# Kernel tuning notes

Measured on AMD Instinct MI355X. Metric: run time of the kernel, lower is better.

Reference implementation:

```python
import jax, jax.numpy as jnp
import numpy as np

VARIANCE = (0.1, 0.2)   # SSD variance from init_kwargs
TOP_K = 1000            # max detections / NMS candidates per (image, class)


def _pairwise_iou(b):
    # b: [K,4] in point form (x1,y1,x2,y2)
    area = jnp.maximum(b[:, 2] - b[:, 0], 0.0) * jnp.maximum(b[:, 3] - b[:, 1], 0.0)
    lt = jnp.maximum(b[:, None, :2], b[None, :, :2])
    rb = jnp.minimum(b[:, None, 2:], b[None, :, 2:])
    wh = jnp.maximum(rb - lt, 0.0)
    inter = wh[..., 0] * wh[..., 1]
    union = area[:, None] + area[None, :] - inter
    return inter / jnp.maximum(union, 1e-12)


def _nms_pack(points, csboxes, scores, conf_thresh, nms_thresh):
    # points/csboxes: [P,4]; scores: [P]. Returns [TOP_K, 5] = (score, cx, cy, w, h)
    K = TOP_K
    masked = jnp.where(scores >= conf_thresh, scores, -jnp.inf)
    vals, idx = jax.lax.top_k(masked, K)          # sorted descending
    p = points[idx]                                # [K,4] point form
    cs = csboxes[idx]                              # [K,4] center-size form
    valid = vals >= conf_thresh
    iou = _pairwise_iou(p)                         # [K,K]
    ar = jnp.arange(K)

    def body(i, keep):
        # box i (if kept) suppresses all lower-scored boxes with IoU > thresh
        sup = (iou[i] > nms_thresh) & (ar > i) & keep[i]
        return keep & ~sup

    keep = jax.lax.fori_loop(0, K, body, valid)
    rows = jnp.concatenate([vals[:, None], cs], axis=1)        # [K,5]
    pos = jnp.where(keep, jnp.cumsum(keep) - 1, K)             # compact kept rows to front
    out = jnp.zeros((K, 5), rows.dtype).at[pos].set(rows, mode='drop')
    return out


def setup_inputs() -> dict:
    key = jax.random.key(0)
    k1, k2, k3, k4 = jax.random.split(key, 4)
    B, P, C = 8, 120000, 5
    loc_data = jax.random.normal(k1, (B, 4, P), dtype=jnp.float32) * 0.5
    conf_data = jax.random.normal(k2, (B, C, P), dtype=jnp.float32)
    cxcy = jax.random.uniform(k3, (P, 2), dtype=jnp.float32)
    wh = 0.01 + 0.29 * jax.random.uniform(k4, (P, 2), dtype=jnp.float32)
    prior_data = jnp.concatenate([cxcy, wh], axis=1)           # (cx,cy,w,h) in [0,1]
    return {
        'loc_data': loc_data,
        'conf_data': conf_data,
        'prior_data': prior_data,
        'conf_thresh': jnp.float32(0.05),
        'nms_thresh': jnp.float32(0.5),
    }


def reference(loc_data, conf_data, prior_data, conf_thresh, nms_thresh):
    v0, v1 = VARIANCE
    # softmax over class dim, drop background class 0 -> [B, Cfg, P]
    conf = jax.nn.softmax(conf_data, axis=1)[:, 1:]
    loc = jnp.transpose(loc_data, (0, 2, 1))                   # [B,P,4]
    # SSD decode -> center-size boxes
    cxcy = prior_data[None, :, :2] + loc[..., :2] * v0 * prior_data[None, :, 2:]
    wh = prior_data[None, :, 2:] * jnp.exp(loc[..., 2:] * v1)
    cs = jnp.concatenate([cxcy, wh], axis=-1)                  # [B,P,4] center-size
    pts = jnp.concatenate([cxcy - wh / 2, cxcy + wh / 2], axis=-1)  # [B,P,4] point form
    per_class = jax.vmap(_nms_pack, in_axes=(None, None, 0, None, None))
    per_image = jax.vmap(per_class, in_axes=(0, 0, 0, None, None))
    return per_image(pts, cs, conf, conf_thresh, nms_thresh)   # [B, Cfg, TOP_K, 5]
```

## Files before the change

kernel.cpp:

```cpp
#include <hip/hip_runtime.h>
#include <cstdint>
#include <cstddef>

typedef unsigned long long ull;

#define KTOP   1000
#define CAP    4096
#define HBITS  14
#define HSHIFT (32 - HBITS)
#define NB2    512
#define BLO    3584
#define ROWS   1024
#define WORDS  16
#define HCH4   2048
#define GSTAGE 4096

__global__ void decode_kernel(const float* __restrict__ conf,
                              float* __restrict__ scores,
                              unsigned* __restrict__ histz,
                              int histW,
                              int B, int C, int P) {
#pragma clang fp contract(off)
    int t = blockIdx.x * blockDim.x + threadIdx.x;

    for (int i = t; i < histW; i += gridDim.x * blockDim.x) histz[i] = 0u;

    if (t >= B * P) return;
    int b = t / P;
    int p = t - b * P;

    float x[8];
    float m = -INFINITY;
    for (int c = 0; c < C; ++c) {
        x[c] = conf[((size_t)b * C + c) * P + p];
        m = fmaxf(m, x[c]);
    }
    float sum = 0.f;
    for (int c = 0; c < C; ++c) {
        x[c] = expf(x[c] - m);
        sum += x[c];
    }
    for (int c = 1; c < C; ++c) {
        float v = x[c] / sum;
        int bc = b * (C - 1) + (c - 1);
        scores[(size_t)bc * P + p] = v;
    }
}

__global__ void __launch_bounds__(256)
hist_kernel(const float* __restrict__ scores,
            const float* __restrict__ cthp,
            unsigned* __restrict__ hist,
            int P) {
    __shared__ unsigned sh[NB2 / 2];
    int bc  = blockIdx.x;
    int tid = threadIdx.x;
    float cth = *cthp;

    sh[tid] = 0u;
    __syncthreads();

    int lo = blockIdx.y * HCH4;
    int hi = lo + HCH4; if (hi > P) hi = P;
    const float* s = scores + (size_t)bc * P;
    const float4* s4 = (const float4*)(s + lo);
    int n4 = (hi - lo) >> 2;
    for (int i = tid; i < n4; i += 256) {
        float4 v4 = s4[i];
        float vv[4] = {v4.x, v4.y, v4.z, v4.w};
        #pragma unroll
        for (int e = 0; e < 4; ++e) {
            float v = vv[e];
            if (v >= cth) {
                int bl = (int)(__float_as_uint(v) >> HSHIFT) - BLO;
                if (bl < 0) bl = 0;
                atomicAdd(&sh[bl >> 1], (bl & 1) ? 65536u : 1u);
            }
        }
    }
    int tl = lo + (n4 << 2);
    for (int p = tl + tid; p < hi; p += 256) {
        float v = s[p];
        if (v >= cth) {
            int bl = (int)(__float_as_uint(v) >> HSHIFT) - BLO;
            if (bl < 0) bl = 0;
            atomicAdd(&sh[bl >> 1], (bl & 1) ? 65536u : 1u);
        }
    }
    __syncthreads();

    unsigned* h = hist + (size_t)bc * NB2;
    unsigned v = sh[tid];
    if (v & 0xFFFFu)  atomicAdd(&h[2 * tid],     v & 0xFFFFu);
    if (v >> 16)      atomicAdd(&h[2 * tid + 1], v >> 16);
}

__global__ void __launch_bounds__(256)
gather_kernel(const float* __restrict__ scores,
              const unsigned* __restrict__ hist,
              unsigned* __restrict__ pivot,
              unsigned* __restrict__ cnt,
              ull* __restrict__ cand,
              const float* __restrict__ cthp, int P) {
    __shared__ ull stage[GSTAGE];
    __shared__ unsigned wpart[4];
    __shared__ unsigned s_pv, l_cnt, s_base;
    int bc = blockIdx.x;
    int tid  = threadIdx.x;
    int wv   = tid >> 6;
    int lane = tid & 63;
    const float* s = scores + (size_t)bc * P;
    float cth = *cthp;

    const unsigned* h = hist + (size_t)bc * NB2;
    unsigned s0 = h[2 * tid], s1 = h[2 * tid + 1];
    unsigned v = s0 + s1;
    if (tid == 0) { s_pv = 0u; l_cnt = 0u; }
    #pragma unroll
    for (int d = 1; d < 64; d <<= 1) {
        unsigned y = (unsigned)__shfl_down((int)v, d);
        if (lane + d < 64) v += y;
    }
    if (lane == 0) wpart[wv] = v;
    __syncthreads();
    unsigned carry = 0;
    for (int w2 = wv + 1; w2 < 4; ++w2) carry += wpart[w2];
    unsigned St = v + carry;
    if (St >= (unsigned)KTOP && (St - s0 - s1) < (unsigned)KTOP) {
        unsigned pl = (St - s0 >= (unsigned)KTOP) ? (2u * tid + 1u) : (2u * tid);
        s_pv = pl + (unsigned)BLO;
    }
    __syncthreads();
    unsigned pv = s_pv;
    if (pv <= (unsigned)BLO) pv = 0u;
    if (blockIdx.y == 0 && tid == 0) pivot[bc] = pv;

    int nchunk = gridDim.y;
    int chunk = (P + nchunk - 1) / nchunk;
    int lo = blockIdx.y * chunk;
    int hi = lo + chunk; if (hi > P) hi = P;

    for (int p0 = lo; p0 < hi; p0 += 256) {
        int p = p0 + tid;
        bool q = false; unsigned k = 0u;
        if (p < hi) {
            float vs = s[p];
            k = __float_as_uint(vs);
            q = (vs >= cth) && ((k >> HSHIFT) >= pv);
        }
        ull mb = __ballot(q);
        if (mb) {
            unsigned wbase = 0u;
            if (lane == 0) wbase = atomicAdd(&l_cnt, (unsigned)__popcll(mb));
            wbase = (unsigned)__shfl((int)wbase, 0);
            if (q) {
                unsigned pos = wbase + (unsigned)__popcll(mb & ((1ull << lane) - 1ull));
                stage[pos] = ((ull)k << 32) | (unsigned)(~(unsigned)p);
            }
        }
    }
    __syncthreads();

    unsigned tot = l_cnt;
    if (tid == 0) s_base = tot ? atomicAdd(&cnt[bc], tot) : 0u;
    __syncthreads();
    unsigned base = s_base;
    ull* cb = cand + (size_t)bc * CAP;
    for (unsigned i = tid; i < tot; i += 256) {
        unsigned off = base + i;
        if (off < CAP) cb[off] = stage[i];
    }
}

__global__ void __launch_bounds__(1024)
sort_kernel(const ull* __restrict__ cand,
            const unsigned* __restrict__ cnt,
            const unsigned* __restrict__ pivot,
            const float* __restrict__ loc,
            const float* __restrict__ prior,
            float* __restrict__ rows,
            float4* __restrict__ pbox,
            float* __restrict__ bar,
            int* __restrict__ nselArr,
            int P, int Cfg) {
#pragma clang fp contract(off)
    int bc  = blockIdx.x;
    int b   = bc / Cfg;
    int tid = threadIdx.x;
    int wv   = tid >> 6;
    int lane = tid & 63;
    __shared__ ull sbuf[CAP];
    __shared__ unsigned h2[1024];
    __shared__ unsigned wpart[16], wcarry[16];
    __shared__ unsigned s_hi, s_spv, s_m2, s_pos;

    int M = (int)cnt[bc]; if (M > CAP) M = CAP;
    int nsel = M < KTOP ? M : KTOP;
    if (tid == 0) nselArr[bc] = nsel;

    for (int i = tid; i < M; i += 1024)
        sbuf[i] = cand[(size_t)bc * CAP + i];
    __syncthreads();

    int Meff = M;
    if (M > 1024) {
        unsigned pv = pivot[bc];
        h2[tid] = 0u;
        if (tid == 0) { s_hi = 0u; s_pos = 0u; s_spv = 0u; s_m2 = (unsigned)M; }
        __syncthreads();
        for (int i = tid; i < M; i += 1024) {
            unsigned sb32 = (unsigned)(sbuf[i] >> 32);
            if ((sb32 >> HSHIFT) > pv) atomicAdd(&s_hi, 1u);
            else atomicAdd(&h2[(sb32 >> 8) & 1023u], 1u);
        }
        __syncthreads();
        unsigned hicnt = s_hi;
        unsigned h0 = h2[tid];
        unsigned v = h0;
        #pragma unroll
        for (int d = 1; d < 64; d <<= 1) {
            unsigned y = (unsigned)__shfl_down((int)v, d);
            if (lane + d < 64) v += y;
        }
        if (lane == 0) wpart[wv] = v;
        __syncthreads();
        if (tid < 16) {
            unsigned c2 = 0;
            for (int w2 = tid + 1; w2 < 16; ++w2) c2 += wpart[w2];
            wcarry[tid] = c2;
        }
        __syncthreads();
        unsigned A  = hicnt + v + wcarry[wv];
        unsigned Bv = A - h0;
        if (A >= (unsigned)KTOP && Bv < (unsigned)KTOP) { s_spv = (unsigned)tid; s_m2 = A; }
        __syncthreads();
        unsigned thr24 = ((unsigned)pv << 10) | s_spv;
        Meff = (int)s_m2;
        ull my[CAP / 1024];
        #pragma unroll
        for (int j = 0; j < CAP / 1024; ++j) { int i = tid + (j << 10); my[j] = (i < M) ? sbuf[i] : 0ull; }
        __syncthreads();
        #pragma unroll
        for (int j = 0; j < CAP / 1024; ++j) {
            int i = tid + (j << 10);
            if (i < M && (unsigned)(my[j] >> 40) >= thr24) {
                unsigned pos = atomicAdd(&s_pos, 1u);
                sbuf[pos] = my[j];
            }
        }
        __syncthreads();
    }

    int n = 1024;
    while (n < Meff) n <<= 1;
    for (int i = tid; i < n; i += 1024)
        if (i >= Meff) sbuf[i] = 0ull;
    __syncthreads();

    for (unsigned k = 2; k <= (unsigned)n; k <<= 1) {
        for (unsigned j = k >> 1; j > 0; j >>= 1) {
            for (unsigned i = tid; i < (unsigned)n; i += 1024) {
                unsigned ixj = i ^ j;
                if (ixj > i) {
                    bool up = ((i & k) == 0u);
                    ull a = sbuf[i], bb = sbuf[ixj];
                    if ((a > bb) == up) { sbuf[i] = bb; sbuf[ixj] = a; }
                }
            }
            __syncthreads();
        }
    }

    for (int r = tid; r < nsel; r += 1024) {
        ull e = sbuf[n - 1 - r];
        float sc = __uint_as_float((unsigned)(e >> 32));
        int idx = (int)(~(unsigned)e);
        float l0 = loc[((size_t)b * 4 + 0) * P + idx];
        float l1 = loc[((size_t)b * 4 + 1) * P + idx];
        float l2 = loc[((size_t)b * 4 + 2) * P + idx];
        float l3 = loc[((size_t)b * 4 + 3) * P + idx];
        float4 pr4 = *(const float4*)(prior + (size_t)idx * 4);
        float cx = pr4.x + (l0 * 0.1f) * pr4.z;
        float cy = pr4.y + (l1 * 0.1f) * pr4.w;
        float w  = pr4.z * expf(l2 * 0.2f);
        float h  = pr4.w * expf(l3 * 0.2f);
        float x1 = cx - w / 2.f, y1 = cy - h / 2.f;
        float x2 = cx + w / 2.f, y2 = cy + h / 2.f;
        size_t sb = (size_t)bc * ROWS + r;
        pbox[sb] = make_float4(x1, y1, x2, y2);
        bar[sb]  = fmaxf(x2 - x1, 0.f) * fmaxf(y2 - y1, 0.f);
        float* rr = rows + ((size_t)bc * KTOP + r) * 5;
        rr[0] = sc; rr[1] = cx; rr[2] = cy; rr[3] = w; rr[4] = h;
    }
}

__global__ void __launch_bounds__(1024)
mask_kernel(const float4* __restrict__ pbox,
            const float* __restrict__ bar,
            const int* __restrict__ nselArr,
            const float* __restrict__ nthp,
            ull* __restrict__ mask) {
#pragma clang fp contract(off)
    int bc   = blockIdx.x;
    int tile = blockIdx.y;
    int tid  = threadIdx.x;
    int nsel = nselArr[bc];
    float nth = *nthp;

    __shared__ float4 sbox[ROWS];
    __shared__ float  sar[ROWS];
    size_t sb = (size_t)bc * ROWS;
    sbox[tid] = pbox[sb + tid];
    sar[tid]  = bar[sb + tid];
    __syncthreads();

    int wv   = tid >> 6;
    int lane = tid & 63;
    int i0   = tile * 64 + (wv << 2);

    ull rowbits[4] = {0ull, 0ull, 0ull, 0ull};
    if (i0 < nsel) {
        float4 bi[4]; float ai[4];
        #pragma unroll
        for (int r = 0; r < 4; ++r) { bi[r] = sbox[i0 + r]; ai[r] = sar[i0 + r]; }

        int whi = (nsel + 63) >> 6; if (whi > WORDS) whi = WORDS;
        for (int w = tile; w < whi; ++w) {
            int j = (w << 6) + lane;
            float4 bj = sbox[j];
            float  aj = sar[j];
            #pragma unroll
            for (int r = 0; r < 4; ++r) {
                int i = i0 + r;
                float ww = fmaxf(fminf(bi[r].z, bj.z) - fmaxf(bi[r].x, bj.x), 0.f);
                float hh = fmaxf(fminf(bi[r].w, bj.w) - fmaxf(bi[r].y, bj.y), 0.f);
                float inter = ww * hh;
                float uni = ai[r] + aj - inter;
                float iou = inter / fmaxf(uni, 1e-12f);
                bool ok = (j > i) && (j < nsel) && (iou > nth);
                ull bits = __ballot(ok);
                if (lane == w) rowbits[r] = bits;
            }
        }
    }
    #pragma unroll
    for (int r = 0; r < 4; ++r)
        if (lane < WORDS)
            mask[(((size_t)bc * ROWS + (i0 + r)) << 4) + lane] = rowbits[r];
}

__device__ __forceinline__ void nms_chunk_body(
    int c, int nchunk, int lane, int g, int w,
    const ull* __restrict__ mrow, ull* sm,
    ull (&pr)[16], ull (&st)[16], ull& S)
{
    int cb = (c & 1) << 10;
    int nb = ((c + 1) & 1) << 10;
    if (c + 2 < nchunk) {
        #pragma unroll
        for (int k = 0; k < 16; ++k)
            pr[k] = mrow[(size_t)(c + 2) * 1024 + k * 64 + lane];
    }

    ull cur = __shfl(S, c);
    ull dbuf[16], dnxt[16];
    #pragma unroll
    for (int k = 0; k < 16; ++k) dbuf[k] = sm[cb + (k << 4) + c];
    #pragma unroll
    for (int grp = 0; grp < 4; ++grp) {
        if (grp < 3) {
            #pragma unroll
            for (int k = 0; k < 16; ++k)
                dnxt[k] = sm[cb + ((((grp + 1) << 4) + k) << 4) + c];
        }
        #pragma unroll
        for (int k = 0; k < 16; ++k) {
            int i = (grp << 4) + k;
            ull supm = (ull)((long long)(cur << (63 - i)) >> 63);
            cur |= dbuf[k] & ~supm;
        }
        if (grp < 3) {
            #pragma unroll
            for (int k = 0; k < 16; ++k) dbuf[k] = dnxt[k];
        }
    }
    ull kbits = ~cur;

    unsigned sub = (unsigned)((kbits >> (g << 4)) & 0xFFFFull);
    int rbase2 = cb + (g << 8) + w;
    ull part = 0ull;
    #pragma unroll
    for (int i = 0; i < 16; ++i) {
        ull v = sm[rbase2 + (i << 4)];
        part |= v & (ull)(0ll - (long long)((sub >> i) & 1u));
    }
    part |= __shfl_xor(part, 16);
    part |= __shfl_xor(part, 32);
    S |= part;
    if (lane == c) S = cur;

    if (c + 1 < nchunk) {
        #pragma unroll
        for (int k = 0; k < 16; ++k) sm[nb + k * 64 + lane] = st[k];
    }
}

__global__ void __launch_bounds__(256)
reduce_pack_kernel(const ull* __restrict__ mask,
                   const int* __restrict__ nselArr,
                   const float* __restrict__ rows,
                   float* __restrict__ out) {
    int bc  = blockIdx.x;
    int tid = threadIdx.x;
    int nsel = nselArr[bc];
    const ull* mrow = mask + ((size_t)bc * ROWS << 4);

    __shared__ ull sm[2048];
    __shared__ ull kw[WORDS];
    __shared__ unsigned pref[WORDS + 1];

    if (tid < 64) {
        int lane = tid;
        int nchunk = (nsel + 63) >> 6;
        ull S = 0ull;
        int g = lane >> 4;
        int w = lane & 15;

        ull ra[16], rb[16];
        if (nchunk > 0) {
            #pragma unroll
            for (int k = 0; k < 16; ++k) ra[k] = mrow[k * 64 + lane];
            if (nchunk > 1) {
                #pragma unroll
                for (int k = 0; k < 16; ++k) rb[k] = mrow[1024 + k * 64 + lane];
            }
            #pragma unroll
            for (int k = 0; k < 16; ++k) sm[k * 64 + lane] = ra[k];

            #pragma unroll 1
            for (int cc = 0; cc < 8; ++cc) {
                int c0 = cc << 1;
                if (c0 >= nchunk) break;
                nms_chunk_body(c0, nchunk, lane, g, w, mrow, sm, ra, rb, S);
                int c1 = c0 + 1;
                if (c1 >= nchunk) break;
                nms_chunk_body(c1, nchunk, lane, g, w, mrow, sm, rb, ra, S);
            }
        }

        if (lane < WORDS) {
            int base_i = lane << 6;
            ull valid = 0ull;
            int rem = nsel - base_i;
            if (rem > 0) valid = (rem >= 64) ? ~0ull : ((1ull << rem) - 1ull);
            kw[lane] = (~S) & valid;
        }
    }
    __syncthreads();

    if (tid == 0) {
        unsigned c = 0;
        for (int w = 0; w < WORDS; ++w) { pref[w] = c; c += (unsigned)__popcll(kw[w]); }
        pref[WORDS] = c;
    }
    __syncthreads();
    unsigned tot = pref[WORDS];

    const float* rbase = rows + (size_t)bc * KTOP * 5;
    float* obase = out + (size_t)bc * KTOP * 5;
    for (int r = tid; r < KTOP; r += 256) {
        ull wv = kw[r >> 6];
        if ((wv >> (r & 63)) & 1ull) {
            int pos = (int)pref[r >> 6] + __popcll(wv & ((1ull << (r & 63)) - 1ull));
            const float* rr = rbase + r * 5;
            float* oo = obase + pos * 5;
            oo[0] = rr[0]; oo[1] = rr[1]; oo[2] = rr[2]; oo[3] = rr[3]; oo[4] = rr[4];
        }
        if (r >= (int)tot) {
            float* oo = obase + r * 5;
            oo[0] = 0.f; oo[1] = 0.f; oo[2] = 0.f; oo[3] = 0.f; oo[4] = 0.f;
        }
    }
}

extern "C" void kernel_launch(void* const* d_in, const int* in_sizes, int n_in,
                              void* d_out, int out_size, void* d_ws, size_t ws_size,
                              hipStream_t stream) {
    (void)n_in; (void)out_size; (void)ws_size;
    const float* loc   = (const float*)d_in[0];
    const float* conf  = (const float*)d_in[1];
    const float* prior = (const float*)d_in[2];
    const float* cth   = (const float*)d_in[3];
    const float* nth   = (const float*)d_in[4];
    float* out = (float*)d_out;

    int P   = in_sizes[2] / 4;
    int B   = in_sizes[0] / (4 * P);
    int C   = in_sizes[1] / (B * P);
    int Cfg = C - 1;
    int NBC = B * Cfg;

    char* base = (char*)d_ws;
    size_t off = 0;
    auto carve = [&](size_t bytes) { char* p = base + off; off = (off + bytes + 255) & ~(size_t)255; return p; };

    float4*   pbox   = (float4*)  carve((size_t)NBC * ROWS * 16);
    ull*      cand   = (ull*)     carve((size_t)NBC * CAP * 8);
    ull*      mask   = (ull*)     carve((size_t)NBC * ROWS * WORDS * 8);
    float*    scores = (float*)   carve((size_t)NBC * P * 4);
    float*    rows   = (float*)   carve((size_t)NBC * KTOP * 5 * 4);
    float*    bar    = (float*)   carve((size_t)NBC * ROWS * 4);
    unsigned* hist   = (unsigned*)carve((size_t)NBC * NB2 * 4 + (size_t)NBC * 4);
    unsigned* cnt    = hist + (size_t)NBC * NB2;
    unsigned* pivot  = (unsigned*)carve((size_t)NBC * 4);
    int*      nselA  = (int*)     carve((size_t)NBC * 4);

    int histW = NBC * NB2 + NBC;

    int GYH = (P + HCH4 - 1) / HCH4;
    int GY = (P + GSTAGE - 1) / GSTAGE;
    if (GY < 32) GY = 32;

    int n1 = B * P;
    decode_kernel<<<(n1 + 255) / 256, 256, 0, stream>>>(conf, scores, hist, histW, B, C, P);
    hist_kernel<<<dim3(NBC, GYH), 256, 0, stream>>>(scores, cth, hist, P);
    gather_kernel<<<dim3(NBC, GY), 256, 0, stream>>>(scores, hist, pivot, cnt, cand, cth, P);
    sort_kernel<<<NBC, 1024, 0, stream>>>(cand, cnt, pivot, loc, prior, rows, pbox, bar, nselA, P, Cfg);
    mask_kernel<<<dim3(NBC, ROWS / 64), 1024, 0, stream>>>(pbox, bar, nselA, nth, mask);
    reduce_pack_kernel<<<NBC, 256, 0, stream>>>(mask, nselA, rows, out);
}
```

Measured before the change: 179.6 us.

## Fuse score histogram into softmax decode and use register bitonic sort

Builds the per-class score histogram inside the softmax decode kernel using shared-memory atomics per class. This removes the separate histogram pass that re-read all scores. Zeroing the histogram moves to a small separate kernel, since decode now writes to it. The sort kernel gains a fast path for up to 1024 candidates: a register-resident bitonic sort that uses 64-bit wave shuffles for small strides and shared memory only for large strides, which cuts the barriers and shared-memory traffic per stage.

```diff
diff --git a/kernel.cpp b/kernel.cpp
--- a/kernel.cpp
+++ b/kernel.cpp
@@ -12,87 +12,64 @@
 #define BLO    3584
 #define ROWS   1024
 #define WORDS  16
-#define HCH4   2048
 #define GSTAGE 4096
 
-__global__ void decode_kernel(const float* __restrict__ conf,
-                              float* __restrict__ scores,
-                              unsigned* __restrict__ histz,
-                              int histW,
-                              int B, int C, int P) {
+__global__ void zero_kernel(unsigned* __restrict__ z, int n) {
+    int t = blockIdx.x * 256 + threadIdx.x;
+    for (int i = t; i < n; i += gridDim.x * 256) z[i] = 0u;
+}
+
+__global__ void __launch_bounds__(256)
+decode_kernel(const float* __restrict__ conf,
+              const float* __restrict__ cthp,
+              float* __restrict__ scores,
+              unsigned* __restrict__ hist,
+              int C, int P) {
 #pragma clang fp contract(off)
-    int t = blockIdx.x * blockDim.x + threadIdx.x;
-
-    for (int i = t; i < histW; i += gridDim.x * blockDim.x) histz[i] = 0u;
-
-    if (t >= B * P) return;
-    int b = t / P;
-    int p = t - b * P;
-
-    float x[8];
-    float m = -INFINITY;
-    for (int c = 0; c < C; ++c) {
-        x[c] = conf[((size_t)b * C + c) * P + p];
-        m = fmaxf(m, x[c]);
-    }
-    float sum = 0.f;
-    for (int c = 0; c < C; ++c) {
-        x[c] = expf(x[c] - m);
-        sum += x[c];
-    }
-    for (int c = 1; c < C; ++c) {
-        float v = x[c] / sum;
-        int bc = b * (C - 1) + (c - 1);
-        scores[(size_t)bc * P + p] = v;
-    }
-}
-
-__global__ void __launch_bounds__(256)
-hist_kernel(const float* __restrict__ scores,
-            const float* __restrict__ cthp,
-            unsigned* __restrict__ hist,
-            int P) {
-    __shared__ unsigned sh[NB2 / 2];
-    int bc  = blockIdx.x;
     int tid = threadIdx.x;
+    int p   = blockIdx.x * 256 + tid;
+    int b   = blockIdx.y;
+    int Cfg = C - 1;
     float cth = *cthp;
 
-    sh[tid] = 0u;
-    __syncthreads();
-
-    int lo = blockIdx.y * HCH4;
-    int hi = lo + HCH4; if (hi > P) hi = P;
-    const float* s = scores + (size_t)bc * P;
-    const float4* s4 = (const float4*)(s + lo);
-    int n4 = (hi - lo) >> 2;
-    for (int i = tid; i < n4; i += 256) {
-        float4 v4 = s4[i];
-        float vv[4] = {v4.x, v4.y, v4.z, v4.w};
-        #pragma unroll
-        for (int e = 0; e < 4; ++e) {
-            float v = vv[e];
+    __shared__ unsigned shh[8 * (NB2 / 2)];
+    for (int i = tid; i < Cfg * (NB2 / 2); i += 256) shh[i] = 0u;
+    __syncthreads();
+
+    if (p < P) {
+        float x[8];
+        float m = -INFINITY;
+        for (int c = 0; c < C; ++c) {
+            x[c] = conf[((size_t)b * C + c) * P + p];
+            m = fmaxf(m, x[c]);
+        }
+        float sum = 0.f;
+        for (int c = 0; c < C; ++c) {
+            x[c] = expf(x[c] - m);
+            sum += x[c];
+        }
+        for (int c = 1; c < C; ++c) {
+            float v = x[c] / sum;
+            scores[((size_t)b * Cfg + (c - 1)) * P + p] = v;
             if (v >= cth) {
                 int bl = (int)(__float_as_uint(v) >> HSHIFT) - BLO;
                 if (bl < 0) bl = 0;
-                atomicAdd(&sh[bl >> 1], (bl & 1) ? 65536u : 1u);
-            }
-        }
-    }
-    int tl = lo + (n4 << 2);
-    for (int p = tl + tid; p < hi; p += 256) {
-        float v = s[p];
-        if (v >= cth) {
-            int bl = (int)(__float_as_uint(v) >> HSHIFT) - BLO;
-            if (bl < 0) bl = 0;
-            atomicAdd(&sh[bl >> 1], (bl & 1) ? 65536u : 1u);
-        }
-    }
-    __syncthreads();
-
-    unsigned* h = hist + (size_t)bc * NB2;
-    unsigned v = sh[tid];
-    if (v & 0xFFFFu)  atomicAdd(&h[2 * tid],     v & 0xFFFFu);
-    if (v >> 16)      atomicAdd(&h[2 * tid + 1], v >> 16);
+                atomicAdd(&shh[(c - 1) * (NB2 / 2) + (bl >> 1)], (bl & 1) ? 65536u : 1u);
+            }
+        }
+    }
+    __syncthreads();
+
+    for (int i = tid; i < Cfg * (NB2 / 2); i += 256) {
+        unsigned v = shh[i];
+        if (v) {
+            int cls  = i >> 8;
+            int word = i & 255;
+            unsigned* h = hist + ((size_t)b * Cfg + cls) * NB2;
+            if (v & 0xFFFFu)  atomicAdd(&h[2 * word],     v & 0xFFFFu);
+            if (v >> 16)      atomicAdd(&h[2 * word + 1], v >> 16);
+        }
+    }
 }
 
 __global__ void __launch_bounds__(256)
@@ -170,6 +147,13 @@
         unsigned off = base + i;
         if (off < CAP) cb[off] = stage[i];
     }
+}
+
+__device__ __forceinline__ ull shfl_xor64(ull v, int m) {
+    unsigned lo = (unsigned)v, hi = (unsigned)(v >> 32);
+    lo = (unsigned)__shfl_xor((int)lo, m);
+    hi = (unsigned)__shfl_xor((int)hi, m);
+    return ((ull)hi << 32) | (ull)lo;
 }
 
 __global__ void __launch_bounds__(1024)
@@ -252,22 +236,46 @@
     }
 
     int n = 1024;
-    while (n < Meff) n <<= 1;
-    for (int i = tid; i < n; i += 1024)
-        if (i >= Meff) sbuf[i] = 0ull;
-    __syncthreads();
-
-    for (unsigned k = 2; k <= (unsigned)n; k <<= 1) {
-        for (unsigned j = k >> 1; j > 0; j >>= 1) {
-            for (unsigned i = tid; i < (unsigned)n; i += 1024) {
-                unsigned ixj = i ^ j;
-                if (ixj > i) {
-                    bool up = ((i & k) == 0u);
-                    ull a = sbuf[i], bb = sbuf[ixj];
-                    if ((a > bb) == up) { sbuf[i] = bb; sbuf[ixj] = a; }
+    if (Meff <= 1024) {
+        ull x = (tid < Meff) ? sbuf[tid] : 0ull;
+        for (unsigned k = 2; k <= 1024u; k <<= 1) {
+            for (unsigned j = k >> 1; j > 0; j >>= 1) {
+                ull p2;
+                if (j >= 64u) {
+                    __syncthreads();
+                    sbuf[tid] = x;
+                    __syncthreads();
+                    p2 = sbuf[tid ^ (int)j];
+                } else {
+                    p2 = shfl_xor64(x, (int)j);
                 }
-            }
-            __syncthreads();
+                bool asc   = (((unsigned)tid & k) == 0u);
+                bool lower = (((unsigned)tid & j) == 0u);
+                ull mn = (x < p2) ? x : p2;
+                ull mx = (x < p2) ? p2 : x;
+                x = (asc == lower) ? mn : mx;
+            }
+        }
+        __syncthreads();
+        sbuf[tid] = x;
+        __syncthreads();
+    } else {
+        while (n < Meff) n <<= 1;
+        for (int i = tid; i < n; i += 1024)
+            if (i >= Meff) sbuf[i] = 0ull;
+        __syncthreads();
+        for (unsigned k = 2; k <= (unsigned)n; k <<= 1) {
+            for (unsigned j = k >> 1; j > 0; j >>= 1) {
+                for (unsigned i = tid; i < (unsigned)n; i += 1024) {
+                    unsigned ixj = i ^ j;
+                    if (ixj > i) {
+                        bool up = ((i & k) == 0u);
+                        ull a = sbuf[i], bb = sbuf[ixj];
+                        if ((a > bb) == up) { sbuf[i] = bb; sbuf[ixj] = a; }
+                    }
+                }
+                __syncthreads();
+            }
         }
     }
 
@@ -517,13 +525,11 @@
 
     int histW = NBC * NB2 + NBC;
 
-    int GYH = (P + HCH4 - 1) / HCH4;
     int GY = (P + GSTAGE - 1) / GSTAGE;
     if (GY < 32) GY = 32;
 
-    int n1 = B * P;
-    decode_kernel<<<(n1 + 255) / 256, 256, 0, stream>>>(conf, scores, hist, histW, B, C, P);
-    hist_kernel<<<dim3(NBC, GYH), 256, 0, stream>>>(scores, cth, hist, P);
+    zero_kernel<<<64, 256, 0, stream>>>(hist, histW);
+    decode_kernel<<<dim3((P + 255) / 256, B), 256, 0, stream>>>(conf, cth, scores, hist, C, P);
     gather_kernel<<<dim3(NBC, GY), 256, 0, stream>>>(scores, hist, pivot, cnt, cand, cth, P);
     sort_kernel<<<NBC, 1024, 0, stream>>>(cand, cnt, pivot, loc, prior, rows, pbox, bar, nselA, P, Cfg);
     mask_kernel<<<dim3(NBC, ROWS / 64), 1024, 0, stream>>>(pbox, bar, nselA, nth, mask);
```

Result: slower. 215.5 us (+20.0%).

## Register-resident bitonic sort with wave shuffles; preload full NMS mask into LDS

Applied to the files above, without the earlier changes.

In the sort kernel, when the candidate count fits in 1024, each thread keeps one key in a register and runs the bitonic network with 64-bit wave shuffles for strides below 64. It uses LDS and block barriers only for larger strides, which removes most of the per-step barriers and LDS round trips. The NMS reduce kernel now loads the whole per-(image,class) mask (up to 128KB) into LDS with all 256 threads up front. This replaces the single-wave double-buffered global prefetch. The extra LDS use lowers occupancy and serializes the load before the scan.

```diff
diff --git a/kernel.cpp b/kernel.cpp
--- a/kernel.cpp
+++ b/kernel.cpp
@@ -170,6 +170,13 @@
         unsigned off = base + i;
         if (off < CAP) cb[off] = stage[i];
     }
+}
+
+__device__ __forceinline__ ull shfl_xor64(ull v, int m) {
+    unsigned lo = (unsigned)v, hi = (unsigned)(v >> 32);
+    lo = (unsigned)__shfl_xor((int)lo, m);
+    hi = (unsigned)__shfl_xor((int)hi, m);
+    return ((ull)hi << 32) | (ull)lo;
 }
 
 __global__ void __launch_bounds__(1024)
@@ -252,22 +259,46 @@
     }
 
     int n = 1024;
-    while (n < Meff) n <<= 1;
-    for (int i = tid; i < n; i += 1024)
-        if (i >= Meff) sbuf[i] = 0ull;
-    __syncthreads();
-
-    for (unsigned k = 2; k <= (unsigned)n; k <<= 1) {
-        for (unsigned j = k >> 1; j > 0; j >>= 1) {
-            for (unsigned i = tid; i < (unsigned)n; i += 1024) {
-                unsigned ixj = i ^ j;
-                if (ixj > i) {
-                    bool up = ((i & k) == 0u);
-                    ull a = sbuf[i], bb = sbuf[ixj];
-                    if ((a > bb) == up) { sbuf[i] = bb; sbuf[ixj] = a; }
+    if (Meff <= 1024) {
+        ull x = (tid < Meff) ? sbuf[tid] : 0ull;
+        for (unsigned k = 2; k <= 1024u; k <<= 1) {
+            for (unsigned j = k >> 1; j > 0; j >>= 1) {
+                ull p2;
+                if (j >= 64u) {
+                    __syncthreads();
+                    sbuf[tid] = x;
+                    __syncthreads();
+                    p2 = sbuf[tid ^ (int)j];
+                } else {
+                    p2 = shfl_xor64(x, (int)j);
                 }
-            }
-            __syncthreads();
+                bool asc   = (((unsigned)tid & k) == 0u);
+                bool lower = (((unsigned)tid & j) == 0u);
+                ull mn = (x < p2) ? x : p2;
+                ull mx = (x < p2) ? p2 : x;
+                x = (asc == lower) ? mn : mx;
+            }
+        }
+        __syncthreads();
+        sbuf[tid] = x;
+        __syncthreads();
+    } else {
+        while (n < Meff) n <<= 1;
+        for (int i = tid; i < n; i += 1024)
+            if (i >= Meff) sbuf[i] = 0ull;
+        __syncthreads();
+        for (unsigned k = 2; k <= (unsigned)n; k <<= 1) {
+            for (unsigned j = k >> 1; j > 0; j >>= 1) {
+                for (unsigned i = tid; i < (unsigned)n; i += 1024) {
+                    unsigned ixj = i ^ j;
+                    if (ixj > i) {
+                        bool up = ((i & k) == 0u);
+                        ull a = sbuf[i], bb = sbuf[ixj];
+                        if ((a > bb) == up) { sbuf[i] = bb; sbuf[ixj] = a; }
+                    }
+                }
+                __syncthreads();
+            }
         }
     }
 
@@ -349,62 +380,6 @@
             mask[(((size_t)bc * ROWS + (i0 + r)) << 4) + lane] = rowbits[r];
 }
 
-__device__ __forceinline__ void nms_chunk_body(
-    int c, int nchunk, int lane, int g, int w,
-    const ull* __restrict__ mrow, ull* sm,
-    ull (&pr)[16], ull (&st)[16], ull& S)
-{
-    int cb = (c & 1) << 10;
-    int nb = ((c + 1) & 1) << 10;
-    if (c + 2 < nchunk) {
-        #pragma unroll
-        for (int k = 0; k < 16; ++k)
-            pr[k] = mrow[(size_t)(c + 2) * 1024 + k * 64 + lane];
-    }
-
-    ull cur = __shfl(S, c);
-    ull dbuf[16], dnxt[16];
-    #pragma unroll
-    for (int k = 0; k < 16; ++k) dbuf[k] = sm[cb + (k << 4) + c];
-    #pragma unroll
-    for (int grp = 0; grp < 4; ++grp) {
-        if (grp < 3) {
-            #pragma unroll
-            for (int k = 0; k < 16; ++k)
-                dnxt[k] = sm[cb + ((((grp + 1) << 4) + k) << 4) + c];
-        }
-        #pragma unroll
-        for (int k = 0; k < 16; ++k) {
-            int i = (grp << 4) + k;
-            ull supm = (ull)((long long)(cur << (63 - i)) >> 63);
-            cur |= dbuf[k] & ~supm;
-        }
-        if (grp < 3) {
-            #pragma unroll
-            for (int k = 0; k < 16; ++k) dbuf[k] = dnxt[k];
-        }
-    }
-    ull kbits = ~cur;
-
-    unsigned sub = (unsigned)((kbits >> (g << 4)) & 0xFFFFull);
-    int rbase2 = cb + (g << 8) + w;
-    ull part = 0ull;
-    #pragma unroll
-    for (int i = 0; i < 16; ++i) {
-        ull v = sm[rbase2 + (i << 4)];
-        part |= v & (ull)(0ll - (long long)((sub >> i) & 1u));
-    }
-    part |= __shfl_xor(part, 16);
-    part |= __shfl_xor(part, 32);
-    S |= part;
-    if (lane == c) S = cur;
-
-    if (c + 1 < nchunk) {
-        #pragma unroll
-        for (int k = 0; k < 16; ++k) sm[nb + k * 64 + lane] = st[k];
-    }
-}
-
 __global__ void __launch_bounds__(256)
 reduce_pack_kernel(const ull* __restrict__ mask,
                    const int* __restrict__ nselArr,
@@ -415,37 +390,59 @@
     int nsel = nselArr[bc];
     const ull* mrow = mask + ((size_t)bc * ROWS << 4);
 
-    __shared__ ull sm[2048];
+    __shared__ ull sm[ROWS * WORDS];
     __shared__ ull kw[WORDS];
     __shared__ unsigned pref[WORDS + 1];
 
+    int nchunk = (nsel + 63) >> 6;
+    int tot_w = nchunk << 10;
+    for (int i = tid; i < tot_w; i += 256) sm[i] = mrow[i];
+    __syncthreads();
+
     if (tid < 64) {
         int lane = tid;
-        int nchunk = (nsel + 63) >> 6;
-        ull S = 0ull;
         int g = lane >> 4;
         int w = lane & 15;
-
-        ull ra[16], rb[16];
-        if (nchunk > 0) {
+        ull S = 0ull;
+
+        for (int c = 0; c < nchunk; ++c) {
+            int base = c << 10;
+            ull cur = __shfl(S, c);
+            ull dbuf[16], dnxt[16];
             #pragma unroll
-            for (int k = 0; k < 16; ++k) ra[k] = mrow[k * 64 + lane];
-            if (nchunk > 1) {
+            for (int k = 0; k < 16; ++k) dbuf[k] = sm[base + (k << 4) + c];
+            #pragma unroll
+            for (int grp = 0; grp < 4; ++grp) {
+                if (grp < 3) {
+                    #pragma unroll
+                    for (int k = 0; k < 16; ++k)
+                        dnxt[k] = sm[base + ((((grp + 1) << 4) + k) << 4) + c];
+                }
                 #pragma unroll
-                for (int k = 0; k < 16; ++k) rb[k] = mrow[1024 + k * 64 + lane];
-            }
+                for (int k = 0; k < 16; ++k) {
+                    int i2 = (grp << 4) + k;
+                    ull supm = (ull)((long long)(cur << (63 - i2)) >> 63);
+                    cur |= dbuf[k] & ~supm;
+                }
+                if (grp < 3) {
+                    #pragma unroll
+                    for (int k = 0; k < 16; ++k) dbuf[k] = dnxt[k];
+                }
+            }
+            ull kbits = ~cur;
+
+            unsigned sub = (unsigned)((kbits >> (g << 4)) & 0xFFFFull);
+            int rbase2 = base + (g << 8) + w;
+            ull part = 0ull;
             #pragma unroll
-            for (int k = 0; k < 16; ++k) sm[k * 64 + lane] = ra[k];
-
-            #pragma unroll 1
-            for (int cc = 0; cc < 8; ++cc) {
-                int c0 = cc << 1;
-                if (c0 >= nchunk) break;
-                nms_chunk_body(c0, nchunk, lane, g, w, mrow, sm, ra, rb, S);
-                int c1 = c0 + 1;
-                if (c1 >= nchunk) break;
-                nms_chunk_body(c1, nchunk, lane, g, w, mrow, sm, rb, ra, S);
-            }
+            for (int i = 0; i < 16; ++i) {
+                ull v = sm[rbase2 + (i << 4)];
+                part |= v & (ull)(0ll - (long long)((sub >> i) & 1u));
+            }
+            part |= __shfl_xor(part, 16);
+            part |= __shfl_xor(part, 32);
+            S |= part;
+            if (lane == c) S = cur;
         }
 
         if (lane < WORDS) {
```

Result: slower. 188.1 us (+4.7%).
